# Kernel optimization log

Measured on AMD Instinct MI355X. Metric: run time of the kernel, lower is better.

The kernel has to match this reference:

```python
import jax, jax.numpy as jnp
import numpy as np

B, S, D = 4, 2048, 1024

def setup_inputs() -> dict:
    key = jax.random.key(0)
    k1, k2, k3, k4 = jax.random.split(key, 4)
    x = jax.random.normal(k1, (B, S, D), dtype=jnp.float32)
    # module init: jr.normal(key, (dim, dim)) / 40
    Qw = jax.random.normal(k2, (D, D), dtype=jnp.float32) / 40
    Kw = jax.random.normal(k3, (D, D), dtype=jnp.float32) / 40
    Vw = jax.random.normal(k4, (D, D), dtype=jnp.float32) / 40
    return {"x": x, "Qw": Qw, "Kw": Kw, "Vw": Vw}

def reference(x, Qw, Kw, Vw):
    # Q/K/V projections: [B,S,D] @ [D,D] -> [B,S,D]
    Q = x @ Qw
    K = x @ Kw
    V = x @ Vw
    d = x.shape[-1]
    S_len = x.shape[-2]
    # causal additive mask: 0 on/below diagonal, -inf above
    mask = jnp.where(jnp.tril(jnp.ones((S_len, S_len), dtype=x.dtype)) == 0,
                     -jnp.inf, 0.0).astype(x.dtype)
    # scores: [B,S,S]
    scores = jnp.einsum('bqd,bkd->bqk', Q, K) / jnp.sqrt(jnp.asarray(d, x.dtype))
    scores = scores + mask
    attn = jax.nn.softmax(scores, axis=-1)
    return jnp.einsum('bqk,bkd->bqd', attn, V)
```

## Files before the change

kernel.cpp:

```cpp
#include <hip/hip_runtime.h>
#include <hip/hip_bf16.h>

typedef __attribute__((ext_vector_type(8))) __bf16 bf16x8;
typedef __attribute__((ext_vector_type(8))) short short8;
typedef __attribute__((ext_vector_type(4))) float f32x4;

#define BK 64

__device__ inline unsigned short f2bf(float f) {
    union { float f; unsigned u; } v; v.f = f;
    unsigned r = (v.u + 0x7FFFu + ((v.u >> 16) & 1u)) >> 16;
    return (unsigned short)r;
}

__device__ __forceinline__ void gld16(const void* g, void* l) {
    __builtin_amdgcn_global_load_lds(
        (const __attribute__((address_space(1))) unsigned int*)g,
        (__attribute__((address_space(3))) unsigned int*)l, 16, 0, 0);
}

__global__ void detect_dtype(const unsigned short* __restrict__ x, int* __restrict__ flag)
{
    const int tid = threadIdx.x;
    int cnt = 0;
    for (int i = tid; i < 1024; i += 256) {
        unsigned e = (x[2 * i] >> 7) & 0xFFu;
        cnt += (e >= 0x60u && e <= 0x88u) ? 1 : 0;
    }
    #pragma unroll
    for (int o = 32; o >= 1; o >>= 1) cnt += __shfl_xor(cnt, o, 64);
    __shared__ int red[4];
    if ((tid & 63) == 0) red[tid >> 6] = cnt;
    __syncthreads();
    if (tid == 0) {
        int t = red[0] + red[1] + red[2] + red[3];
        *flag = (t >= 512) ? 0 : 1;
    }
}

template <int TM>
__global__ __launch_bounds__(256, 2)
void gemm_bt(const unsigned short* __restrict__ A, const unsigned short* __restrict__ Bt,
             void* __restrict__ Call, int K, int lda, int ldb, int ldc,
             long oA, long oB, long oC, long sA, long sB, long sC,
             float scale, int mode, int q0,
             const int* __restrict__ dtf, int outKind,
             const unsigned short* __restrict__ Bt2, void* __restrict__ C2)
{
    constexpr int NI = TM / 32;
    const int dt = *dtf;
    const int z = blockIdx.z;
    if (Bt2 && z) { Bt = Bt2; Call = C2; }
    const long aBase = oA + (long)z * sA;
    const long bBase = oB + (long)z * sB;
    const long cBase = oC + (long)z * sC;

    int mt, nt;
    if (mode == 2) {
        const int nwg2 = gridDim.x * gridDim.y;
        const int h = blockIdx.y * gridDim.x + blockIdx.x;
        const int u = h >> 1;
        const int rank = (h & 1) ? (nwg2 - 1 - u) : u;
        mt = (gridDim.y - 1) - (rank / (int)gridDim.x);
        nt = rank % (int)gridDim.x;
    } else {
        const int nwg = gridDim.x * gridDim.y;
        int lin = blockIdx.y * gridDim.x + blockIdx.x;
        const int q = nwg >> 3, r = nwg & 7;
        const int xcd = lin & 7, idx = lin >> 3;
        lin = (xcd < r ? xcd * (q + 1) : r * (q + 1) + (xcd - r) * q) + idx;
        if (mode == 1) {
            int rem = lin, rr = 0, w = q0 / TM + 1;
            while (rem >= w) { rem -= w; rr++; w++; }
            mt = rr; nt = rem;
        } else { mt = lin / gridDim.x; nt = lin % gridDim.x; }
    }
    const int m0 = mt * TM;
    const int n0 = nt * TM;
    int kmax = K;
    if (mode == 2) kmax = min(K, q0 + m0 + TM);

    __shared__ __align__(16) short As[2][TM * BK];
    __shared__ __align__(16) short Bs[2][TM * BK];

    const int tid  = threadIdx.x;
    const int wave = tid >> 6;
    const int lane = tid & 63;
    const int wm = (wave >> 1) * (TM / 2);
    const int wn = (wave & 1) * (TM / 2);
    const int lrow = lane & 15;
    const int quad = lane >> 4;

    const int sRow = lane >> 3;
    const int sCol = ((lane & 7) ^ sRow) * 8;
    const long gA = aBase + (long)(m0 + wave * (TM / 4) + sRow) * lda + sCol;
    const long gB = bBase + (long)(n0 + wave * (TM / 4) + sRow) * ldb + sCol;

    auto stage = [&](int buf, int k0) {
        short* dA = &As[buf][wave * (TM / 4) * BK];
        short* dB = &Bs[buf][wave * (TM / 4) * BK];
        const unsigned short* pA = A + gA + k0;
        const unsigned short* pB = Bt + gB + k0;
        #pragma unroll
        for (int c = 0; c < TM / 32; c++) {
            gld16(pA + (long)(c * 8) * lda, dA + c * 8 * BK);
            gld16(pB + (long)(c * 8) * ldb, dB + c * 8 * BK);
        }
    };

    f32x4 acc[NI][NI];
    #pragma unroll
    for (int i = 0; i < NI; i++)
        #pragma unroll
        for (int j = 0; j < NI; j++) {
            f32x4 zero = {0.f, 0.f, 0.f, 0.f};
            acc[i][j] = zero;
        }

    const int rq  = lrow & 7;
    const int pc0 = (quad ^ rq) * 8;
    const int pc1 = ((quad + 4) ^ rq) * 8;

    stage(0, 0);
    __syncthreads();
    int cur = 0;

    for (int k0 = 0; k0 < kmax; k0 += BK) {
        const int kn = k0 + BK;
        if (kn < kmax) stage(cur ^ 1, kn);

        const short* rA = &As[cur][0];
        const short* rB = &Bs[cur][0];
        bf16x8 af[NI], bfr[NI];
        #pragma unroll
        for (int i = 0; i < NI; i++) {
            af[i]  = *(const bf16x8*)&rA[(wm + i * 16 + lrow) * BK + pc0];
            bfr[i] = *(const bf16x8*)&rB[(wn + i * 16 + lrow) * BK + pc0];
        }
        #pragma unroll
        for (int i = 0; i < NI; i++)
            #pragma unroll
            for (int j = 0; j < NI; j++)
                acc[i][j] = __builtin_amdgcn_mfma_f32_16x16x32_bf16(af[i], bfr[j], acc[i][j], 0, 0, 0);
        #pragma unroll
        for (int i = 0; i < NI; i++) {
            af[i]  = *(const bf16x8*)&rA[(wm + i * 16 + lrow) * BK + pc1];
            bfr[i] = *(const bf16x8*)&rB[(wn + i * 16 + lrow) * BK + pc1];
        }
        #pragma unroll
        for (int i = 0; i < NI; i++)
            #pragma unroll
            for (int j = 0; j < NI; j++)
                acc[i][j] = __builtin_amdgcn_mfma_f32_16x16x32_bf16(af[i], bfr[j], acc[i][j], 0, 0, 0);

        __syncthreads();
        cur ^= 1;
    }

    const int oF32 = (outKind == 1) | ((outKind == 2) & dt);
    #pragma unroll
    for (int i = 0; i < NI; i++) {
        const int mr = m0 + wm + i * 16 + quad * 4;
        #pragma unroll
        for (int j = 0; j < NI; j++) {
            const int nc = n0 + wn + j * 16 + lrow;
            #pragma unroll
            for (int r = 0; r < 4; r++) {
                const long ofs = cBase + (long)(mr + r) * ldc + nc;
                const float v = acc[i][j][r] * scale;
                if (oF32) ((float*)Call)[ofs] = v;
                else      ((unsigned short*)Call)[ofs] = f2bf(v);
            }
        }
    }
}

__global__ __launch_bounds__(256)
void xpose_cast(const void* __restrict__ src, unsigned short* __restrict__ dT,
                unsigned short* __restrict__ dC, int R, int C,
                long oS, long sS, long sDT, long sDC,
                const int* __restrict__ dtf, int srcExt)
{
    const int dt = srcExt ? *dtf : 0;
    const int b = blockIdx.z;
    const long sb = oS + (long)b * sS;
    __shared__ unsigned short t[64][65];
    const int c0 = blockIdx.x * 64, r0 = blockIdx.y * 64;
    const int tid = threadIdx.x;
    #pragma unroll
    for (int it = 0; it < 16; it++) {
        int idx = it * 256 + tid;
        int r = idx >> 6, c = idx & 63;
        long e = sb + (long)(r0 + r) * C + (c0 + c);
        unsigned short v = dt ? f2bf(((const float*)src)[e]) : ((const unsigned short*)src)[e];
        t[r][c] = v;
        if (dC) dC[(long)b * sDC + (long)(r0 + r) * C + (c0 + c)] = v;
    }
    if (!dT) return;
    __syncthreads();
    #pragma unroll
    for (int it = 0; it < 16; it++) {
        int idx = it * 256 + tid;
        int r = idx >> 6, c = idx & 63;
        dT[(long)b * sDT + (long)(c0 + r) * R + (r0 + c)] = t[c][r];
    }
}

__global__ __launch_bounds__(256)
void cast2(const void* __restrict__ s0, const void* __restrict__ s1,
           unsigned short* __restrict__ d0, unsigned short* __restrict__ d1,
           long n, const int* __restrict__ dtf)
{
    const int dt = *dtf;
    const void* s = blockIdx.y ? s1 : s0;
    unsigned short* d = blockIdx.y ? d1 : d0;
    long i = ((long)blockIdx.x * 256 + threadIdx.x) * 8;
    if (i >= n) return;
    union { short8 v; unsigned short u[8]; } o;
    if (dt) {
        f32x4 a = *(const f32x4*)((const float*)s + i);
        f32x4 b = *(const f32x4*)((const float*)s + i + 4);
        #pragma unroll
        for (int j = 0; j < 4; j++) { o.u[j] = f2bf(a[j]); o.u[4 + j] = f2bf(b[j]); }
    } else {
        o.v = *(const short8*)((const short*)s + i);
    }
    *(short8*)(d + i) = o.v;
}

__global__ __launch_bounds__(256)
void softmax_causal(float* __restrict__ Sc, int S, int CH, int q0)
{
    const int r = blockIdx.x, z = blockIdx.y;
    float* srow = Sc + ((long)z * CH + r) * S;
    unsigned short* prow = (unsigned short*)srow;
    const int n = q0 + r + 1;
    const int limit = q0 + (r & ~127) + 128;
    const int tid = threadIdx.x;
    const int lane = tid & 63, wave = tid >> 6;
    __shared__ float red[4];

    float v[8];
    float lm = -1e30f;
    #pragma unroll
    for (int c = 0; c < 8; c++) {
        int j = c * 256 + tid;
        v[c] = (j < n) ? srow[j] : -1e30f;
        lm = fmaxf(lm, v[c]);
    }
    #pragma unroll
    for (int o = 32; o >= 1; o >>= 1) lm = fmaxf(lm, __shfl_xor(lm, o, 64));
    if (lane == 0) red[wave] = lm;
    __syncthreads();
    const float m = fmaxf(fmaxf(red[0], red[1]), fmaxf(red[2], red[3]));
    __syncthreads();

    float ev[8];
    float ls = 0.f;
    #pragma unroll
    for (int c = 0; c < 8; c++) {
        int j = c * 256 + tid;
        float e = (j < n) ? __expf(v[c] - m) : 0.f;
        ev[c] = e;
        ls += e;
    }
    #pragma unroll
    for (int o = 32; o >= 1; o >>= 1) ls += __shfl_xor(ls, o, 64);
    if (lane == 0) red[wave] = ls;
    __syncthreads();
    const float inv = 1.0f / (red[0] + red[1] + red[2] + red[3]);

    #pragma unroll
    for (int c = 0; c < 8; c++) {
        int j = c * 256 + tid;
        if (j < limit) prow[j] = f2bf(j < n ? ev[c] * inv : 0.f);
    }
}

__global__ __launch_bounds__(256)
void fill_zero(void* o, long n, const int* dtf)
{
    long i = (long)blockIdx.x * 256 + threadIdx.x;
    if (i < n) {
        if (*dtf) ((float*)o)[i] = 0.f;
        else ((unsigned short*)o)[i] = 0;
    }
}

extern "C" void kernel_launch(void* const* d_in, const int* in_sizes, int n_in,
                              void* d_out, int out_size, void* d_ws, size_t ws_size,
                              hipStream_t stream)
{
    const int B = 4, S = 2048, D = 1024;
    const void* x  = d_in[0];
    const void* Qw = d_in[1];
    const void* Kw = d_in[2];
    const void* Vw = d_in[3];
    (void)in_sizes; (void)n_in; (void)out_size;

    int* dtf = (int*)d_ws;
    char* p = (char*)d_ws + 4096;
    const size_t MB = (size_t)1 << 20;
    const unsigned short* nullB = nullptr;

    detect_dtype<<<1, 256, 0, stream>>>((const unsigned short*)x, dtf);

    const long nOut = (long)B * S * D;

    const size_t needA = 4096 + 36 * MB + (size_t)B * S * S * 4;
    if (ws_size >= needA) {
        unsigned short* QwB = (unsigned short*)p;
        unsigned short* KwB = (unsigned short*)(p + 2 * MB);
        unsigned short* Xb  = (unsigned short*)(p + 4 * MB);
        unsigned short* Buf = (unsigned short*)(p + 20 * MB);
        float* Sc = (float*)(p + 36 * MB);
        unsigned short* WT  = (unsigned short*)Sc;
        unsigned short* VwT = QwB;
        unsigned short* VbT = Xb;
        unsigned short* VbS = (unsigned short*)d_out;

        xpose_cast<<<dim3(16, 32, 4), 256, 0, stream>>>(
            x, nullptr, Xb, S, D, 0L, (long)S * D, 0L, (long)S * D, dtf, 1);
        cast2<<<dim3(512, 2), 256, 0, stream>>>(Qw, Kw, QwB, KwB, (long)D * D, dtf);
        gemm_bt<64><<<dim3(16, 16, 1), 256, 0, stream>>>(
            KwB, QwB, WT, D, D, D, D, 0L, 0L, 0L, 0L, 0L, 0L,
            0.03125f, 0, 0, dtf, 0, nullB, nullptr);
        xpose_cast<<<dim3(16, 16, 1), 256, 0, stream>>>(
            Vw, VwT, nullptr, D, D, 0L, 0L, 0L, 0L, dtf, 1);
        gemm_bt<128><<<dim3(8, 64, 2), 256, 0, stream>>>(
            Xb, WT, Buf, D, D, D, D, 0L, 0L, 0L, 0L, 0L, 0L,
            1.0f, 0, 0, dtf, 0, VwT, VbS);
        gemm_bt<128><<<dim3(136, 1, 4), 256, 0, stream>>>(
            Buf, Xb, (void*)Sc, D, D, D, S,
            0L, 0L, 0L, (long)S * D, (long)S * D, (long)S * S,
            1.0f, 1, 0, dtf, 1, nullB, nullptr);
        softmax_causal<<<dim3(S, 4), 256, 0, stream>>>(Sc, S, S, 0);
        xpose_cast<<<dim3(16, 32, 4), 256, 0, stream>>>(
            VbS, VbT, nullptr, S, D, 0L, (long)S * D, (long)D * S, 0L, dtf, 0);
        gemm_bt<128><<<dim3(8, 16, 4), 256, 0, stream>>>(
            (const unsigned short*)Sc, VbT, d_out, S, 2 * S, S, D,
            0L, 0L, 0L, (long)2 * S * S, (long)D * S, (long)S * D,
            1.0f, 2, 0, dtf, 2, nullB, nullptr);
        return;
    }

    const int cfgs[6][2] = {{4,1024},{2,1024},{1,1024},{1,512},{1,256},{1,128}};
    int ZB = 0, CH = 0;
    for (int i = 0; i < 6; i++) {
        size_t need = 4096 + 56 * MB + (size_t)cfgs[i][0] * cfgs[i][1] * S * 4;
        if (need <= ws_size) { ZB = cfgs[i][0]; CH = cfgs[i][1]; break; }
    }
    if (ZB == 0) {
        fill_zero<<<dim3((unsigned)((nOut + 255) / 256)), 256, 0, stream>>>(d_out, nOut, dtf);
        return;
    }

    unsigned short* QwB = (unsigned short*)p;
    unsigned short* KwB = (unsigned short*)(p + 2 * MB);
    unsigned short* WT  = (unsigned short*)(p + 4 * MB);
    unsigned short* VwT = (unsigned short*)(p + 6 * MB);
    unsigned short* Xb  = (unsigned short*)(p + 8 * MB);
    unsigned short* VbT = (unsigned short*)(p + 24 * MB);
    unsigned short* Buf = (unsigned short*)(p + 40 * MB);
    float* Sc = (float*)(p + 56 * MB);
    unsigned short* VbS = (unsigned short*)d_out;

    xpose_cast<<<dim3(16, 32, 4), 256, 0, stream>>>(
        x, nullptr, Xb, S, D, 0L, (long)S * D, 0L, (long)S * D, dtf, 1);
    cast2<<<dim3(512, 2), 256, 0, stream>>>(Qw, Kw, QwB, KwB, (long)D * D, dtf);
    xpose_cast<<<dim3(16, 16, 1), 256, 0, stream>>>(Vw, VwT, nullptr, D, D, 0L, 0L, 0L, 0L, dtf, 1);

    gemm_bt<64><<<dim3(16, 16, 1), 256, 0, stream>>>(
        KwB, QwB, WT, D, D, D, D, 0L, 0L, 0L, 0L, 0L, 0L,
        0.03125f, 0, 0, dtf, 0, nullB, nullptr);
    gemm_bt<128><<<dim3(8, 64, 2), 256, 0, stream>>>(
        Xb, WT, Buf, D, D, D, D, 0L, 0L, 0L, 0L, 0L, 0L,
        1.0f, 0, 0, dtf, 0, VwT, VbS);
    xpose_cast<<<dim3(16, 32, 4), 256, 0, stream>>>(
        VbS, VbT, nullptr, S, D, 0L, (long)S * D, (long)D * S, 0L, dtf, 0);

    for (int b0 = 0; b0 < B; b0 += ZB) {
        for (int q0 = 0; q0 < S; q0 += CH) {
            const int base = q0 / 128, R = CH / 128;
            const int ntiles = R * (base + 1) + R * (R - 1) / 2;

            gemm_bt<128><<<dim3(ntiles, 1, ZB), 256, 0, stream>>>(
                Buf, Xb, (void*)Sc, D, D, D, S,
                (long)b0 * S * D + (long)q0 * D, (long)b0 * S * D, 0L,
                (long)S * D, (long)S * D, (long)CH * S,
                1.0f, 1, q0, dtf, 1, nullB, nullptr);

            softmax_causal<<<dim3(CH, ZB), 256, 0, stream>>>(Sc, S, CH, q0);

            gemm_bt<128><<<dim3(8, CH / 128, ZB), 256, 0, stream>>>(
                (const unsigned short*)Sc, VbT, d_out, S, 2 * S, S, D,
                0L, (long)b0 * D * S, (long)b0 * S * D + (long)q0 * D,
                (long)CH * 2 * S, (long)D * S, (long)S * D,
                1.0f, 2, q0, dtf, 2, nullB, nullptr);
        }
    }
}
```

Baseline: 267.6 us.

## Fuse input casts and Vw transpose into one prep kernel; interleave dual GEMM tiles

Merges the x cast, Qw/Kw casts and the Vw transpose-cast into a single prep kernel, cutting launch count and letting the small jobs share one grid. The dual projection GEMM (X·WT and X·VwT) becomes one 2D grid where odd and even linear tiles alternate between the two B matrices, so both GEMMs share X tiles in cache at the same time. Softmax now loads eight contiguous floats per thread and writes bf16 probabilities with one vector store instead of strided scalar accesses. VwT moves to a separate buffer in the large-workspace path so it no longer aliases QwB, which the fused prep would otherwise race on.

```diff
diff --git a/kernel.cpp b/kernel.cpp
--- a/kernel.cpp
+++ b/kernel.cpp
@@ -35,6 +35,55 @@
     if (tid == 0) {
         int t = red[0] + red[1] + red[2] + red[3];
         *flag = (t >= 512) ? 0 : 1;
+    }
+}
+
+__global__ __launch_bounds__(256)
+void prep(const void* __restrict__ x, const void* __restrict__ Qw,
+          const void* __restrict__ Kw, const void* __restrict__ Vw,
+          unsigned short* __restrict__ Xb, unsigned short* __restrict__ QwB,
+          unsigned short* __restrict__ KwB, unsigned short* __restrict__ VwT,
+          long nX, long nW, int Dd, const int* __restrict__ dtf)
+{
+    const int dt = *dtf;
+    const int bid = blockIdx.x;
+    const int tid = threadIdx.x;
+    const int nbX = (int)(nX >> 11);
+    const int nbW = (int)(nW >> 11);
+    __shared__ unsigned short tbuf[64][65];
+
+    if (bid < nbX + 2 * nbW) {
+        const void* s; unsigned short* d; long i;
+        if (bid < nbX)            { s = x;  d = Xb;  i = ((long)bid << 11) + tid * 8; }
+        else if (bid < nbX + nbW) { s = Qw; d = QwB; i = ((long)(bid - nbX) << 11) + tid * 8; }
+        else                      { s = Kw; d = KwB; i = ((long)(bid - nbX - nbW) << 11) + tid * 8; }
+        union { short8 v; unsigned short u[8]; } o;
+        if (dt) {
+            f32x4 a = *(const f32x4*)((const float*)s + i);
+            f32x4 b = *(const f32x4*)((const float*)s + i + 4);
+            #pragma unroll
+            for (int j = 0; j < 4; j++) { o.u[j] = f2bf(a[j]); o.u[4 + j] = f2bf(b[j]); }
+        } else {
+            o.v = *(const short8*)((const short*)s + i);
+        }
+        *(short8*)(d + i) = o.v;
+        return;
+    }
+    const int t64 = bid - (nbX + 2 * nbW);
+    const int c0 = (t64 & 15) * 64, r0 = (t64 >> 4) * 64;
+    #pragma unroll
+    for (int it = 0; it < 16; it++) {
+        int idx = it * 256 + tid;
+        int r = idx >> 6, c = idx & 63;
+        long e = (long)(r0 + r) * Dd + (c0 + c);
+        tbuf[r][c] = dt ? f2bf(((const float*)Vw)[e]) : ((const unsigned short*)Vw)[e];
+    }
+    __syncthreads();
+    #pragma unroll
+    for (int it = 0; it < 16; it++) {
+        int idx = it * 256 + tid;
+        int r = idx >> 6, c = idx & 63;
+        VwT[(long)(c0 + r) * Dd + (r0 + c)] = tbuf[c][r];
     }
 }
 
@@ -50,7 +99,6 @@
     constexpr int NI = TM / 32;
     const int dt = *dtf;
     const int z = blockIdx.z;
-    if (Bt2 && z) { Bt = Bt2; Call = C2; }
     const long aBase = oA + (long)z * sA;
     const long bBase = oB + (long)z * sB;
     const long cBase = oC + (long)z * sC;
@@ -73,6 +121,10 @@
             int rem = lin, rr = 0, w = q0 / TM + 1;
             while (rem >= w) { rem -= w; rr++; w++; }
             mt = rr; nt = rem;
+        } else if (Bt2) {
+            if (lin & 1) { Bt = Bt2; Call = C2; }
+            const int t = lin >> 1;
+            mt = t >> 3; nt = t & 7;
         } else { mt = lin / gridDim.x; nt = lin % gridDim.x; }
     }
     const int m0 = mt * TM;
@@ -207,28 +259,6 @@
 }
 
 __global__ __launch_bounds__(256)
-void cast2(const void* __restrict__ s0, const void* __restrict__ s1,
-           unsigned short* __restrict__ d0, unsigned short* __restrict__ d1,
-           long n, const int* __restrict__ dtf)
-{
-    const int dt = *dtf;
-    const void* s = blockIdx.y ? s1 : s0;
-    unsigned short* d = blockIdx.y ? d1 : d0;
-    long i = ((long)blockIdx.x * 256 + threadIdx.x) * 8;
-    if (i >= n) return;
-    union { short8 v; unsigned short u[8]; } o;
-    if (dt) {
-        f32x4 a = *(const f32x4*)((const float*)s + i);
-        f32x4 b = *(const f32x4*)((const float*)s + i + 4);
-        #pragma unroll
-        for (int j = 0; j < 4; j++) { o.u[j] = f2bf(a[j]); o.u[4 + j] = f2bf(b[j]); }
-    } else {
-        o.v = *(const short8*)((const short*)s + i);
-    }
-    *(short8*)(d + i) = o.v;
-}
-
-__global__ __launch_bounds__(256)
 void softmax_causal(float* __restrict__ Sc, int S, int CH, int q0)
 {
     const int r = blockIdx.x, z = blockIdx.y;
@@ -238,14 +268,20 @@
     const int limit = q0 + (r & ~127) + 128;
     const int tid = threadIdx.x;
     const int lane = tid & 63, wave = tid >> 6;
+    const int j0 = tid * 8;
     __shared__ float red[4];
 
     float v[8];
+    {
+        f32x4 a = *(const f32x4*)(srow + j0);
+        f32x4 b = *(const f32x4*)(srow + j0 + 4);
+        #pragma unroll
+        for (int c = 0; c < 4; c++) { v[c] = a[c]; v[4 + c] = b[c]; }
+    }
     float lm = -1e30f;
     #pragma unroll
     for (int c = 0; c < 8; c++) {
-        int j = c * 256 + tid;
-        v[c] = (j < n) ? srow[j] : -1e30f;
+        v[c] = (j0 + c < n) ? v[c] : -1e30f;
         lm = fmaxf(lm, v[c]);
     }
     #pragma unroll
@@ -259,8 +295,7 @@
     float ls = 0.f;
     #pragma unroll
     for (int c = 0; c < 8; c++) {
-        int j = c * 256 + tid;
-        float e = (j < n) ? __expf(v[c] - m) : 0.f;
+        float e = (j0 + c < n) ? __expf(v[c] - m) : 0.f;
         ev[c] = e;
         ls += e;
     }
@@ -270,10 +305,11 @@
     __syncthreads();
     const float inv = 1.0f / (red[0] + red[1] + red[2] + red[3]);
 
-    #pragma unroll
-    for (int c = 0; c < 8; c++) {
-        int j = c * 256 + tid;
-        if (j < limit) prow[j] = f2bf(j < n ? ev[c] * inv : 0.f);
+    if (j0 < limit) {
+        union { short8 s; unsigned short u[8]; } o;
+        #pragma unroll
+        for (int c = 0; c < 8; c++) o.u[c] = f2bf(ev[c] * inv);
+        *(short8*)(prow + j0) = o.s;
     }
 }
 
@@ -306,6 +342,9 @@
     detect_dtype<<<1, 256, 0, stream>>>((const unsigned short*)x, dtf);
 
     const long nOut = (long)B * S * D;
+    const long nX = (long)B * S * D;
+    const long nW = (long)D * D;
+    const int prepBlocks = (int)(nX >> 11) + 2 * (int)(nW >> 11) + (D / 64) * (D / 64);
 
     const size_t needA = 4096 + 36 * MB + (size_t)B * S * S * 4;
     if (ws_size >= needA) {
@@ -315,19 +354,16 @@
         unsigned short* Buf = (unsigned short*)(p + 20 * MB);
         float* Sc = (float*)(p + 36 * MB);
         unsigned short* WT  = (unsigned short*)Sc;
-        unsigned short* VwT = QwB;
+        unsigned short* VwT = (unsigned short*)((char*)Sc + 2 * MB);
         unsigned short* VbT = Xb;
         unsigned short* VbS = (unsigned short*)d_out;
 
-        xpose_cast<<<dim3(16, 32, 4), 256, 0, stream>>>(
-            x, nullptr, Xb, S, D, 0L, (long)S * D, 0L, (long)S * D, dtf, 1);
-        cast2<<<dim3(512, 2), 256, 0, stream>>>(Qw, Kw, QwB, KwB, (long)D * D, dtf);
+        prep<<<dim3(prepBlocks), 256, 0, stream>>>(
+            x, Qw, Kw, Vw, Xb, QwB, KwB, VwT, nX, nW, D, dtf);
         gemm_bt<64><<<dim3(16, 16, 1), 256, 0, stream>>>(
             KwB, QwB, WT, D, D, D, D, 0L, 0L, 0L, 0L, 0L, 0L,
             0.03125f, 0, 0, dtf, 0, nullB, nullptr);
-        xpose_cast<<<dim3(16, 16, 1), 256, 0, stream>>>(
-            Vw, VwT, nullptr, D, D, 0L, 0L, 0L, 0L, dtf, 1);
-        gemm_bt<128><<<dim3(8, 64, 2), 256, 0, stream>>>(
+        gemm_bt<128><<<dim3(16, 64, 1), 256, 0, stream>>>(
             Xb, WT, Buf, D, D, D, D, 0L, 0L, 0L, 0L, 0L, 0L,
             1.0f, 0, 0, dtf, 0, VwT, VbS);
         gemm_bt<128><<<dim3(136, 1, 4), 256, 0, stream>>>(
@@ -365,15 +401,12 @@
     float* Sc = (float*)(p + 56 * MB);
     unsigned short* VbS = (unsigned short*)d_out;
 
-    xpose_cast<<<dim3(16, 32, 4), 256, 0, stream>>>(
-        x, nullptr, Xb, S, D, 0L, (long)S * D, 0L, (long)S * D, dtf, 1);
-    cast2<<<dim3(512, 2), 256, 0, stream>>>(Qw, Kw, QwB, KwB, (long)D * D, dtf);
-    xpose_cast<<<dim3(16, 16, 1), 256, 0, stream>>>(Vw, VwT, nullptr, D, D, 0L, 0L, 0L, 0L, dtf, 1);
-
+    prep<<<dim3(prepBlocks), 256, 0, stream>>>(
+        x, Qw, Kw, Vw, Xb, QwB, KwB, VwT, nX, nW, D, dtf);
     gemm_bt<64><<<dim3(16, 16, 1), 256, 0, stream>>>(
         KwB, QwB, WT, D, D, D, D, 0L, 0L, 0L, 0L, 0L, 0L,
         0.03125f, 0, 0, dtf, 0, nullB, nullptr);
-    gemm_bt<128><<<dim3(8, 64, 2), 256, 0, stream>>>(
+    gemm_bt<128><<<dim3(16, 64, 1), 256, 0, stream>>>(
         Xb, WT, Buf, D, D, D, D, 0L, 0L, 0L, 0L, 0L, 0L,
         1.0f, 0, 0, dtf, 0, VwT, VbS);
     xpose_cast<<<dim3(16, 32, 4), 256, 0, stream>>>(
```

Result: faster. 258.5 us (-3.4%).
